# Kernel optimization log

Measured on AMD Instinct MI355X. Metric: run time of the kernel, lower is better.

The kernel has to match this reference:

```python
import jax, jax.numpy as jnp
import numpy as np
from jax import lax

B_J0 = 0.01      # baseline threshold b_j0
BETA = 1.8       # adaptation strength (isAdapt=1)
GAMMA = 0.5      # surrogate-gradient scale
LENS = 0.5       # surrogate-gradient window
TAU_M = 20.0     # membrane time constant
DT = 1.0
HID = 800
OUT = 10
IN = 28
DECODE = 50

@jax.custom_vjp
def act_fun(x):
    # Heaviside spike with rectangular surrogate gradient
    return (x > 0).astype(x.dtype)

def _act_fwd(x):
    return act_fun(x), x

def _act_bwd(x, g):
    return (GAMMA * g * (jnp.abs(x) < LENS).astype(g.dtype),)

act_fun.defvjp(_act_fwd, _act_bwd)

def setup_inputs() -> dict:
    key = jax.random.key(0)
    ks = jax.random.split(key, 8)
    N = 2048
    x = jax.random.normal(ks[0], (N, 784), jnp.float32)
    # xavier-ish init for i2h / h2o, orthogonal-ish scale for h2h
    W_i2h = jax.random.normal(ks[1], (HID, IN), jnp.float32) * (1.0 / np.sqrt(IN))
    b_i2h = jnp.zeros((HID,), jnp.float32)
    W_h2h = jax.random.normal(ks[2], (HID, HID), jnp.float32) * (1.0 / np.sqrt(HID))
    b_h2h = jnp.zeros((HID,), jnp.float32)
    W_h2o = jax.random.normal(ks[3], (OUT, HID), jnp.float32) * (1.0 / np.sqrt(HID))
    b_h2o = jax.random.normal(ks[4], (OUT,), jnp.float32) * 0.01
    tau_adp_h = jnp.full((HID,), 700.0, jnp.float32)
    tau_adp_o = jnp.full((OUT,), 700.0, jnp.float32)
    return {"x": x, "W_i2h": W_i2h, "b_i2h": b_i2h, "W_h2h": W_h2h,
            "b_h2h": b_h2h, "W_h2o": W_h2o, "b_h2o": b_h2o,
            "tau_adp_h": tau_adp_h, "tau_adp_o": tau_adp_o}

def reference(x, W_i2h, b_i2h, W_h2h, b_h2h, W_h2o, b_h2o, tau_adp_h, tau_adp_o):
    N = x.shape[0]
    T = 784 // IN  # 28 encode steps
    # [N, 784] -> [N, IN, T] -> pad 50 zero decode steps -> time-major [T+50, N, IN]
    seq = x.reshape(N, IN, T)
    seq = jnp.concatenate([seq, jnp.zeros((N, IN, DECODE), seq.dtype)], axis=2)
    seq = jnp.transpose(seq, (2, 0, 1))
    alpha = jnp.exp(-DT / jnp.asarray(TAU_M, x.dtype))
    ro_h = jnp.exp(-DT / tau_adp_h)  # [HID]
    ro_o = jnp.exp(-DT / tau_adp_o)  # [OUT]
    mask = (jnp.arange(T + DECODE) >= T).astype(x.dtype)  # accumulate only decode steps

    def step(carry, inp):
        h_mem, h_spk, b_h, o_mem, o_spk, b_o, acc = carry
        xt, m = inp
        # hidden adaptive-LIF update (mem_update_NU_adp)
        h_in = xt @ W_i2h.T + b_i2h + h_spk @ W_h2h.T + b_h2h
        b_h = ro_h * b_h + (1.0 - ro_h) * h_spk
        Bh = B_J0 + BETA * b_h
        h_mem = h_mem * alpha + (1.0 - alpha) * h_in - Bh * h_spk * DT
        h_spk = act_fun(h_mem - Bh)
        # output adaptive-LIF update (mem_update_adp with h2o)
        o_in = h_spk @ W_h2o.T + b_h2o
        b_o = ro_o * b_o + (1.0 - ro_o) * o_spk
        Bo = B_J0 + BETA * b_o
        o_mem = o_mem * alpha + (1.0 - alpha) * o_in - Bo * o_spk * DT
        o_spk = act_fun(o_mem - Bo)
        acc = acc + m * o_spk
        return (h_mem, h_spk, b_h, o_mem, o_spk, b_o, acc), None

    carry0 = (jnp.zeros((N, HID), x.dtype), jnp.zeros((N, HID), x.dtype),
              jnp.full((N, HID), B_J0, x.dtype),
              jnp.zeros((N, OUT), x.dtype), jnp.zeros((N, OUT), x.dtype),
              jnp.full((N, OUT), B_J0, x.dtype),
              jnp.zeros((N, OUT), x.dtype))
    final, _ = lax.scan(step, carry0, (seq, mask))
    return final[6]
```

## Files before the change

kernel.cpp:

```cpp
#include <hip/hip_runtime.h>
#include <math.h>
#include <stdint.h>

namespace {
constexpr int N_    = 2048;
constexpr int H_    = 800;
constexpr int IN_   = 28;
constexpr int TENC  = 28;
constexpr int TTOT  = 78;
constexpr int ONUM  = 10;
constexpr int PODS  = 8;
constexpr int PBLK  = 26;
constexpr int NBLK  = PODS * PBLK;
constexpr int NTILE = 26;
constexpr int BUFD  = NTILE * N_ + 2048;
constexpr int NBUF  = TTOT + 1;
constexpr int FSTR  = 32;
constexpr int NSEG  = 13 * 4 * 2;
constexpr int SMEM_B = NSEG * 1024;
constexpr int SMEM_W = IN_ * 32 * 4;
constexpr int AROW  = 27;
constexpr int SMEM_A = 8 * 32 * AROW * 4;
constexpr int SMEM_TOT = SMEM_B + SMEM_W + SMEM_A;
}

typedef __attribute__((ext_vector_type(4))) int v4i;

__device__ __forceinline__ void digitize(float w, int8_t d[4]) {
    double dd = (double)w * 4294967296.0;
    long long r = (long long)rint(dd);
    int8_t d0 = (int8_t)(r & 255); r = (r - (long long)d0) >> 8;
    int8_t d1 = (int8_t)(r & 255); r = (r - (long long)d1) >> 8;
    int8_t d2 = (int8_t)(r & 255); r = (r - (long long)d2) >> 8;
    long long r3 = r; r3 = r3 > 127 ? 127 : (r3 < -128 ? -128 : r3);
    d[0] = d0; d[1] = d1; d[2] = d2; d[3] = (int8_t)r3;
}

__device__ __forceinline__ v4i unpack16(uint32_t u) {
    v4i f;
    f[0] = (int)((((u      ) & 0xFu) * 0x00204081u) & 0x01010101u);
    f[1] = (int)((((u >>  4) & 0xFu) * 0x00204081u) & 0x01010101u);
    f[2] = (int)((((u >>  8) & 0xFu) * 0x00204081u) & 0x01010101u);
    f[3] = (int)((((u >> 12) & 0xFu) * 0x00204081u) & 0x01010101u);
    return f;
}

__device__ __forceinline__ void pod_barrier(uint32_t* __restrict__ flags,
                                            int pod, int l, uint32_t epoch) {
    __syncthreads();
    if (threadIdx.x < 64) {
        if (threadIdx.x == 0) {
            asm volatile("s_waitcnt vmcnt(0)" ::: "memory");
            __hip_atomic_store(flags + pod * FSTR + l, epoch,
                               __ATOMIC_RELAXED, __HIP_MEMORY_SCOPE_AGENT);
        }
        const bool mine = (threadIdx.x < PBLK);
        bool done = false;
        int itc = 0;
        while (!done) {
            bool ok = true;
            if (mine)
                ok = (__hip_atomic_load(flags + pod * FSTR + threadIdx.x,
                        __ATOMIC_RELAXED, __HIP_MEMORY_SCOPE_AGENT) >= epoch);
            done = (__ballot(ok) == ~0ull);
            if (!done) {
                if (itc < 4) __builtin_amdgcn_s_sleep(1);
                else         __builtin_amdgcn_s_sleep(8);
                ++itc;
            }
        }
    }
    __syncthreads();
}

__global__ void prep_kernel(const float* __restrict__ x, float* __restrict__ xt2,
                            uint32_t* __restrict__ spB, uint32_t* __restrict__ flags)
{
    size_t idx = (size_t)blockIdx.x * blockDim.x + threadIdx.x;
    size_t stride = (size_t)gridDim.x * blockDim.x;
    const size_t TOT = (size_t)TENC * N_ * IN_;
    for (size_t e = idx; e < TOT; e += stride) {
        int t = (int)(e / (N_ * IN_));
        int rem = (int)(e % (N_ * IN_));
        int n = rem / IN_, c = rem % IN_;
        xt2[e] = x[(size_t)n * 784 + c * TENC + t];
    }
    const size_t PW = (size_t)2 * BUFD;
    for (size_t e = idx; e < PW; e += stride) spB[e] = 0u;
    for (size_t e = idx; e < (size_t)PODS * FSTR; e += stride) flags[e] = 0u;
}

__global__ __launch_bounds__(512)
__attribute__((amdgpu_waves_per_eu(2)))
void lsnn_persist(const float* __restrict__ xt2,
                  const float* __restrict__ Wi,
                  const float* __restrict__ b_i2h,
                  const float* __restrict__ Wh,
                  const float* __restrict__ b_h2h,
                  const float* __restrict__ Wo,
                  const float* __restrict__ b_h2o,
                  const float* __restrict__ tau_h,
                  const float* __restrict__ tau_o,
                  uint32_t* spB, int nbuf,
                  uint32_t* flags,
                  float* __restrict__ out)
{
    extern __shared__ __align__(16) int8_t smem[];
    int8_t*   Bl  = smem;
    float*    wl  = (float*)(smem + SMEM_B);
    uint32_t* Alds = (uint32_t*)(smem + SMEM_B + SMEM_W);

    const int bid  = blockIdx.x;
    const int pod  = bid / PBLK;
    const int l    = bid % PBLK;
    const bool is_o = (l == 25);
    const int it   = is_o ? 0 : l;
    const int i0   = it * 32;
    const int wv   = threadIdx.x >> 6;
    const int lane = threadIdx.x & 63;
    const int quad = lane >> 4;
    const int col  = lane & 15;
    const int n0   = pod * 256 + wv * 32;
    uint32_t* ldsA = Alds + wv * 32 * AROW;
    const int dsel = (quad >> 1);
    const int dsh  = (quad & 1) * 16;
    const bool fresh = (nbuf > 2);

    for (int e = threadIdx.x; e < 13 * 2 * 64; e += 512) {
        int c  = e >> 7;
        int bh = (e >> 6) & 1;
        int ln = e & 63;
        int q  = ln >> 4, cl = ln & 15;
        int kbase = c * 64 + q * 16;
        uint32_t w4[4][4] = {};
        int row = bh * 16 + cl;
        #pragma unroll
        for (int j = 0; j < 16; ++j) {
            int kidx = kbase + j;
            float w = 0.f;
            if (kidx < H_) {
                if (!is_o) w = Wh[(size_t)(i0 + row) * H_ + kidx];
                else if (bh == 0 && cl < ONUM) w = Wo[(size_t)cl * H_ + kidx];
            }
            int8_t d[4]; digitize(w, d);
            #pragma unroll
            for (int k = 0; k < 4; ++k)
                w4[k][j >> 2] |= ((uint32_t)(uint8_t)d[k]) << ((j & 3) * 8);
        }
        #pragma unroll
        for (int k = 0; k < 4; ++k) {
            v4i v; v[0] = (int)w4[k][0]; v[1] = (int)w4[k][1];
            v[2] = (int)w4[k][2]; v[3] = (int)w4[k][3];
            *(v4i*)(Bl + (((c * 8) + k * 2 + bh) << 10) + (ln << 4)) = v;
        }
    }
    if (!is_o) {
        for (int e = threadIdx.x; e < IN_ * 32; e += 512) {
            int c = e >> 5, il = e & 31;
            wl[c * 32 + il] = Wi[(size_t)(i0 + il) * IN_ + c];
        }
    }
    if (lane >= 32) ldsA[(lane & 31) * AROW + 25] = 0u;

    const float alpha = (float)exp((double)(-1.0f / 20.0f));
    const float onem  = 1.0f - alpha;
    const double INV32 = 1.0 / 4294967296.0;

    float roB[2] = {}, biB[2] = {}, bhB[2] = {};
    float hm[2][2][4] = {}, hbv[2][2][4];
    float om[2][4] = {}, ospv[2][4] = {}, obb[2][4], cnt[2][4] = {};
    float roO = 0.f, boO = 0.f;
    uint32_t pmask = 0;

    if (!is_o) {
        #pragma unroll
        for (int b = 0; b < 2; ++b) {
            int i = i0 + b * 16 + col;
            float arg = -1.0f / tau_h[i];
            roB[b] = (float)exp((double)arg);
            biB[b] = b_i2h[i]; bhB[b] = b_h2h[i];
        }
        #pragma unroll
        for (int a = 0; a < 2; ++a)
            #pragma unroll
            for (int b = 0; b < 2; ++b)
                #pragma unroll
                for (int r = 0; r < 4; ++r) hbv[a][b][r] = 0.01f;
    } else {
        if (col < ONUM) {
            float arg = -1.0f / tau_o[col];
            roO = (float)exp((double)arg);
            boO = b_h2o[col];
        }
        #pragma unroll
        for (int a = 0; a < 2; ++a)
            #pragma unroll
            for (int r = 0; r < 4; ++r) obb[a][r] = 0.01f;
    }

    uint32_t goff[13]; int loffv[13];
    #pragma unroll
    for (int k = 0; k < 13; ++k) {
        int tile = 2 * k + (lane >> 5);
        goff[k]  = (uint32_t)(tile * N_ + n0 + (lane & 31));
        loffv[k] = (lane & 31) * AROW + tile;
    }
    const int j0 = (lane & 15) * 2;
    const int j1 = j0 + 1;
    const int s0 = ((j0 >> 2) & 3) * 16 + ((j0 >> 4) << 2) + (j0 & 3);
    const int s1 = ((j1 >> 2) & 3) * 16 + ((j1 >> 4) << 2) + (j1 & 3);

    __syncthreads();
    uint32_t epoch = 1;

    for (int t = 0; t <= TTOT; ++t) {
        const uint32_t* rdP = spB + (size_t)(t % nbuf) * BUFD;
        uint32_t*       wrP = spB + (size_t)((t + 1) % nbuf) * BUFD;

        const bool active = is_o ? (t >= 1) : (t < TTOT);

        uint32_t vv[13];
        if (active) {
            if (fresh) {
                #pragma unroll
                for (int k = 0; k < 13; ++k) {
                    const bool real = (k < 12) || (lane < 32);
                    vv[k] = real ? __hip_atomic_load(rdP + goff[k],
                                __ATOMIC_RELAXED, __HIP_MEMORY_SCOPE_WORKGROUP) : 0u;
                }
            } else {
                #pragma unroll
                for (int k = 0; k < 13; ++k) {
                    const bool real = (k < 12) || (lane < 32);
                    vv[k] = real ? __hip_atomic_load(rdP + goff[k],
                                __ATOMIC_RELAXED, __HIP_MEMORY_SCOPE_AGENT) : 0u;
                }
            }
        }

        float inpf[2][2][4] = {};
        if (!is_o && active && t < TENC) {
            #pragma unroll
            for (int a = 0; a < 2; ++a) {
                #pragma unroll
                for (int r = 0; r < 4; ++r) {
                    int n = n0 + a * 16 + quad * 4 + r;
                    const float* xp = xt2 + ((size_t)t * N_ + n) * IN_;
                    double s0d = 0.0, s1d = 0.0;
                    #pragma unroll
                    for (int c = 0; c < IN_; ++c) {
                        double xv = (double)xp[c];
                        s0d += xv * (double)wl[c * 32 + col];
                        s1d += xv * (double)wl[c * 32 + 16 + col];
                    }
                    inpf[a][0][r] = (float)s0d;
                    inpf[a][1][r] = (float)s1d;
                }
            }
        }

        if (active) {
            #pragma unroll
            for (int k = 0; k < 13; ++k) {
                const bool real = (k < 12) || (lane < 32);
                if (real) ldsA[loffv[k]] = vv[k];
            }
        }

        if (!is_o && active) {
            v4i acc4[2][2][4] = {};
            #pragma unroll
            for (int c = 0; c < 13; ++c) {
                uint32_t d0 = ldsA[col * AROW + c * 2 + dsel];
                uint32_t d1 = ldsA[(16 + col) * AROW + c * 2 + dsel];
                v4i a0 = unpack16((d0 >> dsh) & 0xFFFFu);
                v4i a1 = unpack16((d1 >> dsh) & 0xFFFFu);
                #pragma unroll
                for (int k = 0; k < 4; ++k) {
                    v4i b0 = *(const v4i*)(Bl + (((c * 8) + k * 2 + 0) << 10) + (lane << 4));
                    v4i b1 = *(const v4i*)(Bl + (((c * 8) + k * 2 + 1) << 10) + (lane << 4));
                    acc4[0][0][k] = __builtin_amdgcn_mfma_i32_16x16x64_i8(a0, b0, acc4[0][0][k], 0, 0, 0);
                    acc4[0][1][k] = __builtin_amdgcn_mfma_i32_16x16x64_i8(a0, b1, acc4[0][1][k], 0, 0, 0);
                    acc4[1][0][k] = __builtin_amdgcn_mfma_i32_16x16x64_i8(a1, b0, acc4[1][0][k], 0, 0, 0);
                    acc4[1][1][k] = __builtin_amdgcn_mfma_i32_16x16x64_i8(a1, b1, acc4[1][1][k], 0, 0, 0);
                }
            }

            uint32_t nmask = 0;
            {
                #pragma clang fp contract(off)
                #pragma unroll
                for (int a = 0; a < 2; ++a) {
                    #pragma unroll
                    for (int b = 0; b < 2; ++b) {
                        #pragma unroll
                        for (int r = 0; r < 4; ++r) {
                            int sidx = ((a * 2 + b) * 4 + r);
                            int64_t tot = ((int64_t)acc4[a][b][3][r] << 24)
                                        + ((int64_t)acc4[a][b][2][r] << 16)
                                        + ((int64_t)acc4[a][b][1][r] << 8)
                                        +  (int64_t)acc4[a][b][0][r];
                            float rec = (float)((double)tot * INV32);
                            float h_in = ((inpf[a][b][r] + biB[b]) + rec) + bhB[b];
                            float sp = (pmask >> sidx) & 1u ? 1.0f : 0.0f;
                            float ro = roB[b];
                            float bnew = (ro * hbv[a][b][r]) + ((1.0f - ro) * sp);
                            float B = 0.01f + (1.8f * bnew);
                            float mem = ((hm[a][b][r] * alpha) + (onem * h_in)) - (B * sp);
                            float s = (mem - B) > 0.f ? 1.f : 0.f;
                            hbv[a][b][r] = bnew; hm[a][b][r] = mem;
                            if (s > 0.5f) nmask |= (1u << sidx);
                        }
                    }
                }
            }
            pmask = nmask;

            uint32_t wmine = 0;
            #pragma unroll
            for (int a = 0; a < 2; ++a) {
                #pragma unroll
                for (int r = 0; r < 4; ++r) {
                    unsigned long long bal0 = __ballot((nmask >> (a * 8 + r)) & 1u);
                    unsigned long long bal1 = __ballot((nmask >> (a * 8 + 4 + r)) & 1u);
                    if (col == a * 4 + r) {
                        wmine = (uint32_t)((bal0 >> (quad * 16)) & 0xFFFFull)
                              | ((uint32_t)((bal1 >> (quad * 16)) & 0xFFFFull) << 16);
                    }
                }
            }
            {
                uint32_t g0 = (uint32_t)__shfl((int)wmine, s0, 64);
                uint32_t g1 = (uint32_t)__shfl((int)wmine, s1, 64);
                if (lane < 16) {
                    uint64_t q = (uint64_t)g0 | ((uint64_t)g1 << 32);
                    uint64_t* qp = (uint64_t*)(wrP + (size_t)it * N_ + n0);
                    __hip_atomic_store(qp + (lane & 15), q,
                                       __ATOMIC_RELAXED, __HIP_MEMORY_SCOPE_AGENT);
                }
            }
        }

        if (is_o && active) {
            v4i oacc[2][4] = {};
            #pragma unroll
            for (int c = 0; c < 13; ++c) {
                uint32_t d0 = ldsA[col * AROW + c * 2 + dsel];
                uint32_t d1 = ldsA[(16 + col) * AROW + c * 2 + dsel];
                v4i a0 = unpack16((d0 >> dsh) & 0xFFFFu);
                v4i a1 = unpack16((d1 >> dsh) & 0xFFFFu);
                #pragma unroll
                for (int k = 0; k < 4; ++k) {
                    v4i bo = *(const v4i*)(Bl + (((c * 8) + k * 2 + 0) << 10) + (lane << 4));
                    oacc[0][k] = __builtin_amdgcn_mfma_i32_16x16x64_i8(a0, bo, oacc[0][k], 0, 0, 0);
                    oacc[1][k] = __builtin_amdgcn_mfma_i32_16x16x64_i8(a1, bo, oacc[1][k], 0, 0, 0);
                }
            }
            if (col < ONUM) {
                #pragma clang fp contract(off)
                const bool msk = (t - 1) >= TENC;
                #pragma unroll
                for (int a = 0; a < 2; ++a) {
                    #pragma unroll
                    for (int r = 0; r < 4; ++r) {
                        int64_t tot = ((int64_t)oacc[a][3][r] << 24)
                                    + ((int64_t)oacc[a][2][r] << 16)
                                    + ((int64_t)oacc[a][1][r] << 8)
                                    +  (int64_t)oacc[a][0][r];
                        float o_in = ((float)((double)tot * INV32)) + boO;
                        float osp_ = ospv[a][r];
                        float bnew = (roO * obb[a][r]) + ((1.0f - roO) * osp_);
                        float B = 0.01f + (1.8f * bnew);
                        float mem = ((om[a][r] * alpha) + (onem * o_in)) - (B * osp_);
                        float s = (mem - B) > 0.f ? 1.f : 0.f;
                        obb[a][r] = bnew; om[a][r] = mem; ospv[a][r] = s;
                        if (msk) cnt[a][r] += s;
                    }
                }
            }
        }

        if (t < TTOT) pod_barrier(flags, pod, l, epoch++);
    }

    if (is_o && col < ONUM) {
        #pragma unroll
        for (int a = 0; a < 2; ++a)
            #pragma unroll
            for (int r = 0; r < 4; ++r) {
                int n = n0 + a * 16 + quad * 4 + r;
                out[(size_t)n * ONUM + col] = cnt[a][r];
            }
    }
}

extern "C" void kernel_launch(void* const* d_in, const int* in_sizes, int n_in,
                              void* d_out, int out_size, void* d_ws, size_t ws_size,
                              hipStream_t stream)
{
    const float* x      = (const float*)d_in[0];
    const float* Wi     = (const float*)d_in[1];
    const float* b_i2h  = (const float*)d_in[2];
    const float* Wh     = (const float*)d_in[3];
    const float* b_h2h  = (const float*)d_in[4];
    const float* Wo     = (const float*)d_in[5];
    const float* b_h2o  = (const float*)d_in[6];
    const float* tau_h  = (const float*)d_in[7];
    const float* tau_o  = (const float*)d_in[8];
    float* out = (float*)d_out;

    uintptr_t p = (uintptr_t)d_ws;
    auto alloc = [&](size_t bytes) -> void* {
        p = (p + 255) & ~(uintptr_t)255;
        void* r = (void*)p; p += bytes; return r;
    };
    float*    xt2   = (float*)alloc((size_t)TENC * N_ * IN_ * 4);
    uint32_t* flags = (uint32_t*)alloc((size_t)PODS * FSTR * 4);

    uintptr_t used = (p + 255 & ~(uintptr_t)255) - (uintptr_t)d_ws;
    size_t bufbytes = (size_t)BUFD * 4;
    int nbuf = (ws_size >= used + (size_t)NBUF * bufbytes + 4096) ? NBUF : 2;
    uint32_t* spB = (uint32_t*)alloc((size_t)nbuf * bufbytes);

    prep_kernel<<<1024, 256, 0, stream>>>(x, xt2, spB, flags);

    (void)hipFuncSetAttribute((const void*)lsnn_persist,
                              hipFuncAttributeMaxDynamicSharedMemorySize, SMEM_TOT);
    lsnn_persist<<<NBLK, 512, SMEM_TOT, stream>>>(
        xt2, Wi, b_i2h, Wh, b_h2h, Wo, b_h2o, tau_h, tau_o,
        spB, nbuf, flags, out);
}
```

Measured before the change: 1.239 ms.

## Replace per-step pod barrier with tagged spike words polled by consumers

Each 32-bit spike word is now stored as a 64-bit value whose upper half carries the timestep tag. When per-timestep buffers are available (fresh mode), consumers spin on the tags of the exact words they need instead of passing a full pod-wide flag barrier every step. This removes the global barrier round-trip and lets blocks proceed as soon as their inputs are ready. The cost is doubled spike-buffer traffic and footprint, plus retry polling loops on stale words.

```diff
diff --git a/kernel.cpp b/kernel.cpp
--- a/kernel.cpp
+++ b/kernel.cpp
@@ -13,7 +13,7 @@
 constexpr int PBLK  = 26;
 constexpr int NBLK  = PODS * PBLK;
 constexpr int NTILE = 26;
-constexpr int BUFD  = NTILE * N_ + 2048;
+constexpr int BUFQ  = NTILE * N_ + 256;
 constexpr int NBUF  = TTOT + 1;
 constexpr int FSTR  = 32;
 constexpr int NSEG  = 13 * 4 * 2;
@@ -74,7 +74,7 @@
 }
 
 __global__ void prep_kernel(const float* __restrict__ x, float* __restrict__ xt2,
-                            uint32_t* __restrict__ spB, uint32_t* __restrict__ flags)
+                            uint64_t* __restrict__ spB, uint32_t* __restrict__ flags)
 {
     size_t idx = (size_t)blockIdx.x * blockDim.x + threadIdx.x;
     size_t stride = (size_t)gridDim.x * blockDim.x;
@@ -85,8 +85,8 @@
         int n = rem / IN_, c = rem % IN_;
         xt2[e] = x[(size_t)n * 784 + c * TENC + t];
     }
-    const size_t PW = (size_t)2 * BUFD;
-    for (size_t e = idx; e < PW; e += stride) spB[e] = 0u;
+    const size_t PW = (size_t)2 * BUFQ;
+    for (size_t e = idx; e < PW; e += stride) spB[e] = 0ull;
     for (size_t e = idx; e < (size_t)PODS * FSTR; e += stride) flags[e] = 0u;
 }
 
@@ -101,7 +101,7 @@
                   const float* __restrict__ b_h2o,
                   const float* __restrict__ tau_h,
                   const float* __restrict__ tau_o,
-                  uint32_t* spB, int nbuf,
+                  uint64_t* spB, int nbuf,
                   uint32_t* flags,
                   float* __restrict__ out)
 {
@@ -198,42 +198,40 @@
             for (int r = 0; r < 4; ++r) obb[a][r] = 0.01f;
     }
 
-    uint32_t goff[13]; int loffv[13];
+    int goff[13]; int loffv[13];
     #pragma unroll
     for (int k = 0; k < 13; ++k) {
         int tile = 2 * k + (lane >> 5);
-        goff[k]  = (uint32_t)(tile * N_ + n0 + (lane & 31));
+        goff[k]  = tile * N_ + n0 + (lane & 31);
         loffv[k] = (lane & 31) * AROW + tile;
     }
-    const int j0 = (lane & 15) * 2;
-    const int j1 = j0 + 1;
-    const int s0 = ((j0 >> 2) & 3) * 16 + ((j0 >> 4) << 2) + (j0 & 3);
-    const int s1 = ((j1 >> 2) & 3) * 16 + ((j1 >> 4) << 2) + (j1 & 3);
+    const int jrow = lane & 31;
+    const int src  = ((jrow >> 2) & 3) * 16 + ((jrow >> 4) << 2) + (jrow & 3);
 
     __syncthreads();
     uint32_t epoch = 1;
 
     for (int t = 0; t <= TTOT; ++t) {
-        const uint32_t* rdP = spB + (size_t)(t % nbuf) * BUFD;
-        uint32_t*       wrP = spB + (size_t)((t + 1) % nbuf) * BUFD;
+        const uint64_t* rdQ = spB + (size_t)(fresh ? t : (t & 1)) * BUFQ;
+        uint64_t*       wrQ = spB + (size_t)(fresh ? (t + 1) : ((t + 1) & 1)) * BUFQ;
 
         const bool active = is_o ? (t >= 1) : (t < TTOT);
 
-        uint32_t vv[13];
+        uint64_t vv[13];
         if (active) {
             if (fresh) {
                 #pragma unroll
                 for (int k = 0; k < 13; ++k) {
                     const bool real = (k < 12) || (lane < 32);
-                    vv[k] = real ? __hip_atomic_load(rdP + goff[k],
-                                __ATOMIC_RELAXED, __HIP_MEMORY_SCOPE_WORKGROUP) : 0u;
+                    vv[k] = real ? __hip_atomic_load(rdQ + goff[k],
+                                __ATOMIC_RELAXED, __HIP_MEMORY_SCOPE_WORKGROUP) : 0ull;
                 }
             } else {
                 #pragma unroll
                 for (int k = 0; k < 13; ++k) {
                     const bool real = (k < 12) || (lane < 32);
-                    vv[k] = real ? __hip_atomic_load(rdP + goff[k],
-                                __ATOMIC_RELAXED, __HIP_MEMORY_SCOPE_AGENT) : 0u;
+                    vv[k] = real ? __hip_atomic_load(rdQ + goff[k],
+                                __ATOMIC_RELAXED, __HIP_MEMORY_SCOPE_AGENT) : 0ull;
                 }
             }
         }
@@ -260,10 +258,33 @@
         }
 
         if (active) {
+            if (fresh) {
+                int tries = 0;
+                while (true) {
+                    uint32_t fail = 0;
+                    #pragma unroll
+                    for (int k = 0; k < 13; ++k) {
+                        const bool real = (k < 12) || (lane < 32);
+                        if (real && (uint32_t)(vv[k] >> 32) != (uint32_t)t)
+                            fail |= (1u << k);
+                    }
+                    if (__ballot(fail != 0) == 0ull) break;
+                    if      (tries < 4)  __builtin_amdgcn_s_sleep(1);
+                    else if (tries < 10) __builtin_amdgcn_s_sleep(4);
+                    else                 __builtin_amdgcn_s_sleep(16);
+                    ++tries;
+                    #pragma unroll
+                    for (int k = 0; k < 13; ++k) {
+                        if (fail & (1u << k))
+                            vv[k] = __hip_atomic_load(rdQ + goff[k],
+                                        __ATOMIC_RELAXED, __HIP_MEMORY_SCOPE_AGENT);
+                    }
+                }
+            }
             #pragma unroll
             for (int k = 0; k < 13; ++k) {
                 const bool real = (k < 12) || (lane < 32);
-                if (real) ldsA[loffv[k]] = vv[k];
+                if (real) ldsA[loffv[k]] = (uint32_t)vv[k];
             }
         }
 
@@ -330,12 +351,10 @@
                 }
             }
             {
-                uint32_t g0 = (uint32_t)__shfl((int)wmine, s0, 64);
-                uint32_t g1 = (uint32_t)__shfl((int)wmine, s1, 64);
-                if (lane < 16) {
-                    uint64_t q = (uint64_t)g0 | ((uint64_t)g1 << 32);
-                    uint64_t* qp = (uint64_t*)(wrP + (size_t)it * N_ + n0);
-                    __hip_atomic_store(qp + (lane & 15), q,
+                uint32_t myw = (uint32_t)__shfl((int)wmine, src, 64);
+                if (lane < 32) {
+                    uint64_t q = ((uint64_t)(uint32_t)(t + 1) << 32) | (uint64_t)myw;
+                    __hip_atomic_store(wrQ + (size_t)it * N_ + n0 + jrow, q,
                                        __ATOMIC_RELAXED, __HIP_MEMORY_SCOPE_AGENT);
                 }
             }
@@ -380,7 +399,7 @@
             }
         }
 
-        if (t < TTOT) pod_barrier(flags, pod, l, epoch++);
+        if (!fresh && t < TTOT) pod_barrier(flags, pod, l, epoch++);
     }
 
     if (is_o && col < ONUM) {
@@ -417,10 +436,10 @@
     float*    xt2   = (float*)alloc((size_t)TENC * N_ * IN_ * 4);
     uint32_t* flags = (uint32_t*)alloc((size_t)PODS * FSTR * 4);
 
-    uintptr_t used = (p + 255 & ~(uintptr_t)255) - (uintptr_t)d_ws;
-    size_t bufbytes = (size_t)BUFD * 4;
+    uintptr_t used = ((p + 255) & ~(uintptr_t)255) - (uintptr_t)d_ws;
+    size_t bufbytes = (size_t)BUFQ * 8;
     int nbuf = (ws_size >= used + (size_t)NBUF * bufbytes + 4096) ? NBUF : 2;
-    uint32_t* spB = (uint32_t*)alloc((size_t)nbuf * bufbytes);
+    uint64_t* spB = (uint64_t*)alloc((size_t)nbuf * bufbytes);
 
     prep_kernel<<<1024, 256, 0, stream>>>(x, xt2, spB, flags);
 
```

Measured after the change: 1.168 ms. 5.7% less time.
